# Performance work log

Measured on AMD Instinct MI355X. Metric: run time of the kernel, lower is better.

The kernel has to match this reference:

```python
import jax, jax.numpy as jnp
import numpy as np

B, S, H = 2, 2048, 2048
N = 16               # num heads
NOPE, ROPE, V = 128, 64, 128
QHD = NOPE + ROPE    # 192 per-head q/k dim
QL, KVL = 1536, 512  # q_lora_rank, kv_lora_rank
THETA = 10000.0
SCALE = QHD ** -0.5
EPS = 1e-6


def rmsnorm(x, w):
    var = jnp.mean(x.astype(jnp.float32) ** 2, axis=-1, keepdims=True)
    return (x.astype(jnp.float32) * jax.lax.rsqrt(var + EPS)).astype(x.dtype) * w


def rotate_half(x):
    d = x.shape[-1] // 2
    return jnp.concatenate([-x[..., d:], x[..., :d]], axis=-1)


def setup_inputs() -> dict:
    key = jax.random.key(0)
    ks = jax.random.split(key, 8)
    w = lambda k, shape: jax.random.normal(k, shape, jnp.float32) * 0.02
    return {
        "hidden_states": jax.random.normal(ks[0], (B, S, H), jnp.float32),
        "position_ids": (jnp.arange(B * S, dtype=jnp.int64) % 4096).reshape(B, S),
        "q_a_w": w(ks[1], (QL, H)),
        "q_a_ln_w": jnp.ones((QL,), jnp.float32),
        "q_b_w": w(ks[2], (N * QHD, QL)),
        "kv_a_w": w(ks[3], (KVL + ROPE, H)),
        "kv_a_ln_w": jnp.ones((KVL,), jnp.float32),
        "kv_b_w": w(ks[4], (N * (NOPE + V), KVL)),
        "o_w": w(ks[5], (H, N * V)),
    }


def mla_forward(hidden_states, position_ids, q_a_w, q_a_ln_w, q_b_w,
                kv_a_w, kv_a_ln_w, kv_b_w, o_w):
    b, s, _ = hidden_states.shape
    # ---- Q low-rank path: q_b(rmsnorm(q_a(x))) ----
    q = rmsnorm(hidden_states @ q_a_w.T, q_a_ln_w) @ q_b_w.T
    q = q.reshape(b, s, N, QHD)
    q_nope, q_pe = q[..., :NOPE], q[..., NOPE:]
    # ---- compressed KV + shared rope key ----
    kv_a = hidden_states @ kv_a_w.T                       # [b,s,KVL+ROPE]
    compressed_kv = rmsnorm(kv_a[..., :KVL], kv_a_ln_w)   # [b,s,KVL]
    k_pe = kv_a[..., KVL:].reshape(b, s, 1, ROPE)         # MQA rope key
    # ---- RoPE (default, theta=1e4) from position_ids ----
    inv_freq = 1.0 / (THETA ** (jnp.arange(0, ROPE, 2, dtype=jnp.float32) / ROPE))
    freqs = position_ids.astype(jnp.float32)[..., None] * inv_freq  # [b,s,ROPE/2]
    emb = jnp.concatenate([freqs, freqs], axis=-1)                  # [b,s,ROPE]
    cos = jnp.cos(emb)[:, :, None, :].astype(hidden_states.dtype)   # [b,s,1,ROPE]
    sin = jnp.sin(emb)[:, :, None, :].astype(hidden_states.dtype)
    q_pe = q_pe * cos + rotate_half(q_pe) * sin
    k_pe = k_pe * cos + rotate_half(k_pe) * sin
    # ---- decompress latent KV via kv_b_proj ----
    kv = (compressed_kv @ kv_b_w.T).reshape(b, s, N, NOPE + V)
    k_nope, v = kv[..., :NOPE], kv[..., NOPE:]
    k = jnp.concatenate([k_nope, jnp.broadcast_to(k_pe, (b, s, N, ROPE))], axis=-1)
    qf = jnp.concatenate([q_nope, q_pe], axis=-1)          # [b,s,N,QHD]
    # ---- causal SDPA in bsnd layout ----
    scores = jnp.einsum('bqnd,bknd->bnqk', qf, k) * SCALE  # [b,N,s,s]
    causal = jnp.tril(jnp.ones((s, s), bool))
    scores = jnp.where(causal, scores, jnp.finfo(scores.dtype).min)
    probs = jax.nn.softmax(scores, axis=-1)
    attn = jnp.einsum('bnqk,bknd->bqnd', probs, v)         # [b,s,N,V]
    out = attn.reshape(b, s, N * V) @ o_w.T
    return out


def reference(hidden_states, position_ids, q_a_w, q_a_ln_w, q_b_w,
              kv_a_w, kv_a_ln_w, kv_b_w, o_w):
    return mla_forward(hidden_states, position_ids, q_a_w, q_a_ln_w, q_b_w,
                       kv_a_w, kv_a_ln_w, kv_b_w, o_w)
```

## Files before the change

kernel.cpp:

```cpp
#include <hip/hip_runtime.h>
#include <cstdio>

typedef unsigned short u16;
typedef u16 u16x4 __attribute__((ext_vector_type(4)));
typedef u16 u16x8 __attribute__((ext_vector_type(8)));
typedef __bf16 bf16x8 __attribute__((ext_vector_type(8)));
typedef float f32x4 __attribute__((ext_vector_type(4)));

#define AS1 __attribute__((address_space(1)))
#define AS3 __attribute__((address_space(3)))

#define GLOAD16(gsrc, ldst) __builtin_amdgcn_global_load_lds( \
    (const AS1 void*)(gsrc), (AS3 void*)(ldst), 16, 0, 0)

__device__ __forceinline__ u16 f2bf(float f) {
  unsigned u = __builtin_bit_cast(unsigned, f);
  u += 0x7fffu + ((u >> 16) & 1u);
  return (u16)(u >> 16);
}
__device__ __forceinline__ float bf2f(u16 h) {
  return __builtin_bit_cast(float, (unsigned)h << 16);
}

__global__ __launch_bounds__(256) void cvt_pad_k(const float* __restrict__ src,
                                                 u16* __restrict__ dst,
                                                 long srcN, long dstN) {
  long i = ((long)blockIdx.x * 256 + threadIdx.x) * 8;
  const long stride = (long)gridDim.x * 256 * 8;
  for (; i < dstN; i += stride) {
    u16x8 o = {0,0,0,0,0,0,0,0};
    if (i < srcN) {
      const float4* p = (const float4*)(src + i);
      float4 a = p[0], b = p[1];
      o[0]=f2bf(a.x); o[1]=f2bf(a.y); o[2]=f2bf(a.z); o[3]=f2bf(a.w);
      o[4]=f2bf(b.x); o[5]=f2bf(b.y); o[6]=f2bf(b.z); o[7]=f2bf(b.w);
    }
    *(u16x8*)(dst + i) = o;
  }
}

__global__ __launch_bounds__(256) void rms_k(const u16* __restrict__ src, u16* __restrict__ dst,
                                             const float* __restrict__ w,
                                             int sstride, int dstride, int cols) {
  const int row = blockIdx.x;
  const int tid = threadIdx.x;
  const int nch = cols >> 3;
  float x[8];
  float ss = 0.f;
  if (tid < nch) {
    u16x8 v = *(const u16x8*)(src + (size_t)row * sstride + tid * 8);
#pragma unroll
    for (int j = 0; j < 8; ++j) { x[j] = bf2f(v[j]); ss += x[j] * x[j]; }
  } else {
#pragma unroll
    for (int j = 0; j < 8; ++j) x[j] = 0.f;
  }
#pragma unroll
  for (int off = 1; off < 64; off <<= 1) ss += __shfl_xor(ss, off);
  __shared__ float red[4];
  const int wv = tid >> 6, ln = tid & 63;
  if (ln == 0) red[wv] = ss;
  __syncthreads();
  const float tot = red[0] + red[1] + red[2] + red[3];
  const float rs = 1.0f / sqrtf(tot / (float)cols + 1e-6f);
  if (tid < nch) {
    u16x8 o;
#pragma unroll
    for (int j = 0; j < 8; ++j) o[j] = f2bf(x[j] * rs * w[tid * 8 + j]);
    *(u16x8*)(dst + (size_t)row * dstride + tid * 8) = o;
  }
}

__global__ void rope_k(u16* __restrict__ q, const u16* __restrict__ kva,
                       u16* __restrict__ kpe, const int* __restrict__ pos) {
  const int tok = blockIdx.x;
  const int j = threadIdx.x;
  const float p = (float)pos[tok];
  const int jj = j & 31;
  const float inv = __powf(10000.0f, -(float)jj * (1.0f / 32.0f));
  float s, c;
  __sincosf(p * inv, &s, &c);
  const float sgn = (j < 32) ? -1.0f : 1.0f;
  const int partner = (j < 32) ? j + 32 : j - 32;
  {
    const float x  = bf2f(kva[(size_t)tok * 640 + 512 + j]);
    const float xp = bf2f(kva[(size_t)tok * 640 + 512 + partner]);
    kpe[(size_t)tok * 64 + j] = f2bf(x * c + sgn * xp * s);
  }
#pragma unroll
  for (int h = 0; h < 16; ++h) {
    const size_t base = (size_t)tok * 3072 + h * 192 + 128;
    const float x  = bf2f(q[base + j]);
    const float xp = bf2f(q[base + partner]);
    q[base + j] = f2bf(x * c + sgn * xp * s);
  }
}

__global__ __launch_bounds__(256) void gemm_bt(const u16* __restrict__ A, const u16* __restrict__ B,
                                               u16* __restrict__ Cb, float* __restrict__ Cf,
                                               int M, int N, int K) {
  __shared__ __attribute__((aligned(16))) u16 As[128 * 64];
  __shared__ __attribute__((aligned(16))) u16 Bs[128 * 64];
  const int tid = threadIdx.x;
  const int m0 = blockIdx.y * 128, n0 = blockIdx.x * 128;
  const int w = tid >> 6, lane = tid & 63;
  const int wr = w >> 1, wc = w & 1;
  const int lr = lane & 15, g = lane >> 4;

  f32x4 acc[4][4] = {};

  for (int k0 = 0; k0 < K; k0 += 64) {
#pragma unroll
    for (int i = 0; i < 4; ++i) {
      const int c = i * 256 + tid;
      const int row = c >> 3, col = (c & 7) << 3;
      GLOAD16(A + (size_t)(m0 + row) * K + k0 + col, &As[c * 8]);
    }
#pragma unroll
    for (int i = 0; i < 4; ++i) {
      const int c = i * 256 + tid;
      const int row = c >> 3, col = (c & 7) << 3;
      GLOAD16(B + (size_t)(n0 + row) * K + k0 + col, &Bs[c * 8]);
    }
    __syncthreads();
    bf16x8 af[4][2], bfr[4][2];
#pragma unroll
    for (int x = 0; x < 4; ++x)
#pragma unroll
      for (int kk = 0; kk < 2; ++kk) {
        af[x][kk]  = *(const bf16x8*)(&As[(wr * 64 + x * 16 + lr) * 64 + kk * 32 + g * 8]);
        bfr[x][kk] = *(const bf16x8*)(&Bs[(wc * 64 + x * 16 + lr) * 64 + kk * 32 + g * 8]);
      }
#pragma unroll
    for (int mi = 0; mi < 4; ++mi)
#pragma unroll
      for (int ni = 0; ni < 4; ++ni)
#pragma unroll
        for (int kk = 0; kk < 2; ++kk)
          acc[mi][ni] = __builtin_amdgcn_mfma_f32_16x16x32_bf16(af[mi][kk], bfr[ni][kk],
                                                                acc[mi][ni], 0, 0, 0);
    __syncthreads();
  }

  const int rb = m0 + wr * 64, cb = n0 + wc * 64;
#pragma unroll
  for (int mi = 0; mi < 4; ++mi)
#pragma unroll
    for (int ni = 0; ni < 4; ++ni)
#pragma unroll
      for (int i = 0; i < 4; ++i) {
        const int r = rb + mi * 16 + g * 4 + i;
        const int cI = cb + ni * 16 + lr;
        if (Cf) Cf[(size_t)r * N + cI] = acc[mi][ni][i];
        else    Cb[(size_t)r * N + cI] = f2bf(acc[mi][ni][i]);
      }
}

__global__ __launch_bounds__(256) void attn_k(const u16* __restrict__ q, const u16* __restrict__ kvb,
                                              const u16* __restrict__ kpe, u16* __restrict__ ao) {
  __shared__ __attribute__((aligned(16))) u16 Ks[64 * 192];
  __shared__ __attribute__((aligned(16))) u16 Vt[128 * 64];
  __shared__ __attribute__((aligned(16))) u16 Ps[4][32 * 72];

  const float SCALE = 0.07216878364870323f;
  const int bh = blockIdx.x;
  const int b = bh >> 4, h = bh & 15;
  const int j = 15 - blockIdx.y;
  const int tid = threadIdx.x, w = tid >> 6, lane = tid & 63;
  const int lr = lane & 15, g = lane >> 4;

  const int q0 = j * 128;
  const int qrb = q0 + w * 32;

  bf16x8 qf[2][6];
#pragma unroll
  for (int m = 0; m < 2; ++m)
#pragma unroll
    for (int kd = 0; kd < 6; ++kd)
      qf[m][kd] = *(const bf16x8*)(q + (size_t)(b * 2048 + qrb + m * 16 + lr) * 3072 +
                                   h * 192 + kd * 32 + g * 8);

  float mrow[2][4], lrow[2][4];
  f32x4 o[2][8] = {};
#pragma unroll
  for (int m = 0; m < 2; ++m)
#pragma unroll
    for (int i = 0; i < 4; ++i) { mrow[m][i] = -1e30f; lrow[m][i] = 0.f; }

  const int nt = (q0 >> 6) + 2;
  for (int t = 0; t < nt; ++t) {
    const int k0 = t * 64;
#pragma unroll
    for (int i = 0; i < 6; ++i) {
      const int c = i * 256 + tid;
      const int row = c / 24, cl = c - row * 24;
      const int cg = cl ^ (row & 7);
      const u16* src = (cg < 16)
        ? (kvb + (size_t)(b * 2048 + k0 + row) * 4096 + h * 256 + cg * 8)
        : (kpe + (size_t)(b * 2048 + k0 + row) * 64 + (cg - 16) * 8);
      GLOAD16(src, &Ks[c * 8]);
    }
    {
      const int kq = tid >> 4;
      const int vc = (tid & 15) << 3;
      u16x8 vv[4];
#pragma unroll
      for (int r = 0; r < 4; ++r)
        vv[r] = *(const u16x8*)(kvb + (size_t)(b * 2048 + k0 + kq * 4 + r) * 4096 + h * 256 + 128 + vc);
#pragma unroll
      for (int e = 0; e < 8; ++e) {
        const int v = vc + e;
        const int cx = (kq >> 1) ^ (v & 7) ^ ((v >> 3) & 7);
        u16x4 tq = {vv[0][e], vv[1][e], vv[2][e], vv[3][e]};
        *(u16x4*)(&Vt[v * 64 + cx * 8 + (kq & 1) * 4]) = tq;
      }
    }
    __syncthreads();

    if (k0 <= qrb + 31) {
      f32x4 sAcc[2][4] = {};
#pragma unroll
      for (int nf = 0; nf < 4; ++nf) {
        const int rr = nf * 16 + lr;
#pragma unroll
        for (int kd = 0; kd < 6; ++kd) {
          const int ch = (kd * 4 + g) ^ (rr & 7);
          const bf16x8 kf = *(const bf16x8*)(&Ks[rr * 192 + ch * 8]);
#pragma unroll
          for (int m = 0; m < 2; ++m)
            sAcc[m][nf] = __builtin_amdgcn_mfma_f32_16x16x32_bf16(qf[m][kd], kf, sAcc[m][nf], 0, 0, 0);
        }
      }

#pragma unroll
      for (int m = 0; m < 2; ++m) {
        float sv[4][4];
#pragma unroll
        for (int nf = 0; nf < 4; ++nf)
#pragma unroll
          for (int i = 0; i < 4; ++i) {
            const int qrow = qrb + m * 16 + g * 4 + i;
            const int kcol = k0 + nf * 16 + lr;
            const float vS = sAcc[m][nf][i] * SCALE;
            sv[nf][i] = (kcol > qrow) ? -1e30f : vS;
          }
        float fac[4], mn[4];
#pragma unroll
        for (int i = 0; i < 4; ++i) {
          float rm = fmaxf(fmaxf(sv[0][i], sv[1][i]), fmaxf(sv[2][i], sv[3][i]));
          rm = fmaxf(rm, __shfl_xor(rm, 1));
          rm = fmaxf(rm, __shfl_xor(rm, 2));
          rm = fmaxf(rm, __shfl_xor(rm, 4));
          rm = fmaxf(rm, __shfl_xor(rm, 8));
          mn[i] = fmaxf(mrow[m][i], rm);
          fac[i] = __expf(mrow[m][i] - mn[i]);
          mrow[m][i] = mn[i];
        }
#pragma unroll
        for (int i = 0; i < 4; ++i) {
          float rsum = 0.f;
#pragma unroll
          for (int nf = 0; nf < 4; ++nf) { sv[nf][i] = __expf(sv[nf][i] - mn[i]); rsum += sv[nf][i]; }
          rsum += __shfl_xor(rsum, 1);
          rsum += __shfl_xor(rsum, 2);
          rsum += __shfl_xor(rsum, 4);
          rsum += __shfl_xor(rsum, 8);
          lrow[m][i] = lrow[m][i] * fac[i] + rsum;
        }
#pragma unroll
        for (int nv = 0; nv < 8; ++nv)
#pragma unroll
          for (int i = 0; i < 4; ++i) o[m][nv][i] *= fac[i];
#pragma unroll
        for (int nf = 0; nf < 4; ++nf)
#pragma unroll
          for (int i = 0; i < 4; ++i)
            Ps[w][(m * 16 + g * 4 + i) * 72 + nf * 16 + lr] = f2bf(sv[nf][i]);
      }
      asm volatile("s_waitcnt lgkmcnt(0)" ::: "memory");

#pragma unroll
      for (int kc = 0; kc < 2; ++kc) {
        bf16x8 vfr[8];
#pragma unroll
        for (int nv = 0; nv < 8; ++nv) {
          const int v = nv * 16 + lr;
          const int cx = (kc * 4 + g) ^ (v & 7) ^ ((v >> 3) & 7);
          vfr[nv] = *(const bf16x8*)(&Vt[v * 64 + cx * 8]);
        }
#pragma unroll
        for (int m = 0; m < 2; ++m) {
          const bf16x8 pf = *(const bf16x8*)(&Ps[w][(m * 16 + lr) * 72 + kc * 32 + g * 8]);
#pragma unroll
          for (int nv = 0; nv < 8; ++nv)
            o[m][nv] = __builtin_amdgcn_mfma_f32_16x16x32_bf16(pf, vfr[nv], o[m][nv], 0, 0, 0);
        }
      }
    }
    __syncthreads();
  }

#pragma unroll
  for (int m = 0; m < 2; ++m)
#pragma unroll
    for (int i = 0; i < 4; ++i) {
      const float inv = 1.0f / lrow[m][i];
      const size_t tokOff = (size_t)(b * 2048 + qrb + m * 16 + g * 4 + i) * 2048 + h * 128;
#pragma unroll
      for (int nv = 0; nv < 8; ++nv)
        ao[tokOff + nv * 16 + lr] = f2bf(o[m][nv][i] * inv);
    }
}

extern "C" void kernel_launch(void* const* d_in, const int* in_sizes, int n_in,
                              void* d_out, int out_size, void* d_ws, size_t ws_size,
                              hipStream_t stream) {
  const float* hidden  = (const float*)d_in[0];
  const int*   pos     = (const int*)d_in[1];
  const float* q_a_w   = (const float*)d_in[2];
  const float* q_a_ln  = (const float*)d_in[3];
  const float* q_b_w   = (const float*)d_in[4];
  const float* kv_a_w  = (const float*)d_in[5];
  const float* kv_a_ln = (const float*)d_in[6];
  const float* kv_b_w  = (const float*)d_in[7];
  const float* o_w     = (const float*)d_in[8];
  float* out = (float*)d_out;

  char* ws = (char*)d_ws;
  u16* hb  = (u16*)(ws + 0L);
  u16* w1  = (u16*)(ws + 16777216L);
  u16* w2  = (u16*)(ws + 23068672L);
  u16* w3  = (u16*)(ws + 32505856L);
  u16* w4  = (u16*)(ws + 35127296L);
  u16* w5  = (u16*)(ws + 39321600L);
  u16* qa  = (u16*)(ws + 47710208L);
  u16* qb  = (u16*)(ws + 60293120L);
  u16* kva = (u16*)(ws + 85458944L);
  u16* ckv = (u16*)(ws + 90701824L);
  u16* kpe = (u16*)(ws + 94896128L);
  u16* kvb = (u16*)(ws + 95420416L);
  u16* ao  = (u16*)(ws + 128974848L);
  if (ws_size < 145752064UL) { fprintf(stderr, "ws too small: %zu\n", ws_size); return; }

  auto cvt = [&](const float* s, u16* d, long sn, long dn) {
    long blocks = (dn / 8 + 255) / 256; if (blocks > 2048) blocks = 2048;
    cvt_pad_k<<<dim3((unsigned)blocks), dim3(256), 0, stream>>>(s, d, sn, dn);
  };
  cvt(hidden, hb, 4096L * 2048, 4096L * 2048);
  cvt(q_a_w,  w1, 1536L * 2048, 1536L * 2048);
  cvt(q_b_w,  w2, 3072L * 1536, 3072L * 1536);
  cvt(kv_a_w, w3, 576L * 2048,  640L * 2048);
  cvt(kv_b_w, w4, 4096L * 512,  4096L * 512);
  cvt(o_w,    w5, 2048L * 2048, 2048L * 2048);

  gemm_bt<<<dim3(12, 32), 256, 0, stream>>>(hb, w1, qa, nullptr, 4096, 1536, 2048);
  rms_k<<<4096, 256, 0, stream>>>(qa, qa, q_a_ln, 1536, 1536, 1536);
  gemm_bt<<<dim3(24, 32), 256, 0, stream>>>(qa, w2, qb, nullptr, 4096, 3072, 1536);
  gemm_bt<<<dim3(5, 32), 256, 0, stream>>>(hb, w3, kva, nullptr, 4096, 640, 2048);
  rms_k<<<4096, 256, 0, stream>>>(kva, ckv, kv_a_ln, 640, 512, 512);
  rope_k<<<4096, 64, 0, stream>>>(qb, kva, kpe, pos);
  gemm_bt<<<dim3(32, 32), 256, 0, stream>>>(ckv, w4, kvb, nullptr, 4096, 4096, 512);
  attn_k<<<dim3(32, 16), 256, 0, stream>>>(qb, kvb, kpe, ao);
  gemm_bt<<<dim3(16, 32), 256, 0, stream>>>(ao, w5, nullptr, out, 4096, 2048, 2048);
}
```

Before: 481.0 us.

## Register-prefetch next K/V tile in attention, lazy softmax rescale, wider rope blocks

The attention kernel now loads the next K/V tile into registers while the current tile is being computed, then writes it to LDS at the top of the next iteration. This replaces the direct global-to-LDS loads and one of the two barriers per tile, hiding global load latency behind the math. It also skips the online-softmax rescale of the output and row sum unless some row max grows by more than 8, and it asks for two blocks per SM via launch bounds. Separately, rope_k uses 256 threads per token, with the heads split across four waves. The trade-offs are more register pressure and possible spills, since the prefetch keeps ten extra 16-byte vectors live per thread.

```diff
diff --git a/kernel.cpp b/kernel.cpp
--- a/kernel.cpp
+++ b/kernel.cpp
@@ -71,10 +71,11 @@
   }
 }
 
-__global__ void rope_k(u16* __restrict__ q, const u16* __restrict__ kva,
-                       u16* __restrict__ kpe, const int* __restrict__ pos) {
+__global__ __launch_bounds__(256) void rope_k(u16* __restrict__ q, const u16* __restrict__ kva,
+                                              u16* __restrict__ kpe, const int* __restrict__ pos) {
   const int tok = blockIdx.x;
-  const int j = threadIdx.x;
+  const int j = threadIdx.x & 63;
+  const int w = threadIdx.x >> 6;
   const float p = (float)pos[tok];
   const int jj = j & 31;
   const float inv = __powf(10000.0f, -(float)jj * (1.0f / 32.0f));
@@ -82,13 +83,14 @@
   __sincosf(p * inv, &s, &c);
   const float sgn = (j < 32) ? -1.0f : 1.0f;
   const int partner = (j < 32) ? j + 32 : j - 32;
-  {
+  if (w == 0) {
     const float x  = bf2f(kva[(size_t)tok * 640 + 512 + j]);
     const float xp = bf2f(kva[(size_t)tok * 640 + 512 + partner]);
     kpe[(size_t)tok * 64 + j] = f2bf(x * c + sgn * xp * s);
   }
 #pragma unroll
-  for (int h = 0; h < 16; ++h) {
+  for (int hh = 0; hh < 4; ++hh) {
+    const int h = w * 4 + hh;
     const size_t base = (size_t)tok * 3072 + h * 192 + 128;
     const float x  = bf2f(q[base + j]);
     const float xp = bf2f(q[base + partner]);
@@ -156,8 +158,8 @@
       }
 }
 
-__global__ __launch_bounds__(256) void attn_k(const u16* __restrict__ q, const u16* __restrict__ kvb,
-                                              const u16* __restrict__ kpe, u16* __restrict__ ao) {
+__global__ __launch_bounds__(256, 2) void attn_k(const u16* __restrict__ q, const u16* __restrict__ kvb,
+                                                 const u16* __restrict__ kpe, u16* __restrict__ ao) {
   __shared__ __attribute__((aligned(16))) u16 Ks[64 * 192];
   __shared__ __attribute__((aligned(16))) u16 Vt[128 * 64];
   __shared__ __attribute__((aligned(16))) u16 Ps[4][32 * 72];
@@ -180,6 +182,34 @@
       qf[m][kd] = *(const bf16x8*)(q + (size_t)(b * 2048 + qrb + m * 16 + lr) * 3072 +
                                    h * 192 + kd * 32 + g * 8);
 
+  const u16* kptr[6];
+  int kld[6], kstep[6];
+#pragma unroll
+  for (int i = 0; i < 6; ++i) {
+    const int c = i * 256 + tid;
+    const int row = c / 24, cl = c - row * 24;
+    kld[i] = (row * 24 + (cl ^ (row & 7))) * 8;
+    if (cl < 16) { kptr[i] = kvb + (size_t)(b * 2048 + row) * 4096 + h * 256 + cl * 8;
+                   kstep[i] = 64 * 4096; }
+    else         { kptr[i] = kpe + (size_t)(b * 2048 + row) * 64 + (cl - 16) * 8;
+                   kstep[i] = 64 * 64; }
+  }
+  const int kq = tid >> 4, vc = (tid & 15) << 3;
+  const u16* vptr = kvb + (size_t)(b * 2048 + kq * 4) * 4096 + h * 256 + 128 + vc;
+  int vld[8];
+#pragma unroll
+  for (int e = 0; e < 8; ++e) {
+    const int v = vc + e;
+    const int cx = (kq >> 1) ^ (v & 7) ^ ((v >> 3) & 7);
+    vld[e] = v * 64 + cx * 8 + (kq & 1) * 4;
+  }
+
+  u16x8 kreg[6], vreg[4];
+#define LOAD_TILE() do { \
+    _Pragma("unroll") for (int i = 0; i < 6; ++i) kreg[i] = *(const u16x8*)kptr[i]; \
+    _Pragma("unroll") for (int r = 0; r < 4; ++r) vreg[r] = *(const u16x8*)(vptr + r * 4096); \
+  } while (0)
+
   float mrow[2][4], lrow[2][4];
   f32x4 o[2][8] = {};
 #pragma unroll
@@ -188,34 +218,27 @@
     for (int i = 0; i < 4; ++i) { mrow[m][i] = -1e30f; lrow[m][i] = 0.f; }
 
   const int nt = (q0 >> 6) + 2;
+  LOAD_TILE();
+
   for (int t = 0; t < nt; ++t) {
     const int k0 = t * 64;
-#pragma unroll
-    for (int i = 0; i < 6; ++i) {
-      const int c = i * 256 + tid;
-      const int row = c / 24, cl = c - row * 24;
-      const int cg = cl ^ (row & 7);
-      const u16* src = (cg < 16)
-        ? (kvb + (size_t)(b * 2048 + k0 + row) * 4096 + h * 256 + cg * 8)
-        : (kpe + (size_t)(b * 2048 + k0 + row) * 64 + (cg - 16) * 8);
-      GLOAD16(src, &Ks[c * 8]);
-    }
-    {
-      const int kq = tid >> 4;
-      const int vc = (tid & 15) << 3;
-      u16x8 vv[4];
-#pragma unroll
-      for (int r = 0; r < 4; ++r)
-        vv[r] = *(const u16x8*)(kvb + (size_t)(b * 2048 + k0 + kq * 4 + r) * 4096 + h * 256 + 128 + vc);
-#pragma unroll
-      for (int e = 0; e < 8; ++e) {
-        const int v = vc + e;
-        const int cx = (kq >> 1) ^ (v & 7) ^ ((v >> 3) & 7);
-        u16x4 tq = {vv[0][e], vv[1][e], vv[2][e], vv[3][e]};
-        *(u16x4*)(&Vt[v * 64 + cx * 8 + (kq & 1) * 4]) = tq;
-      }
-    }
-    __syncthreads();
+    __builtin_amdgcn_s_barrier();
+#pragma unroll
+    for (int i = 0; i < 6; ++i) *(u16x8*)(&Ks[kld[i]]) = kreg[i];
+#pragma unroll
+    for (int e = 0; e < 8; ++e) {
+      u16x4 tq = {vreg[0][e], vreg[1][e], vreg[2][e], vreg[3][e]};
+      *(u16x4*)(&Vt[vld[e]]) = tq;
+    }
+    if (t + 1 < nt) {
+#pragma unroll
+      for (int i = 0; i < 6; ++i) kptr[i] += kstep[i];
+      vptr += 64 * 4096;
+      LOAD_TILE();
+    }
+    asm volatile("s_waitcnt lgkmcnt(0)" ::: "memory");
+    __builtin_amdgcn_s_barrier();
+    __builtin_amdgcn_sched_barrier(0);
 
     if (k0 <= qrb + 31) {
       f32x4 sAcc[2][4] = {};
@@ -244,7 +267,8 @@
             const float vS = sAcc[m][nf][i] * SCALE;
             sv[nf][i] = (kcol > qrow) ? -1e30f : vS;
           }
-        float fac[4], mn[4];
+        float rm4[4];
+        bool exceed = false;
 #pragma unroll
         for (int i = 0; i < 4; ++i) {
           float rm = fmaxf(fmaxf(sv[0][i], sv[1][i]), fmaxf(sv[2][i], sv[3][i]));
@@ -252,25 +276,31 @@
           rm = fmaxf(rm, __shfl_xor(rm, 2));
           rm = fmaxf(rm, __shfl_xor(rm, 4));
           rm = fmaxf(rm, __shfl_xor(rm, 8));
-          mn[i] = fmaxf(mrow[m][i], rm);
-          fac[i] = __expf(mrow[m][i] - mn[i]);
-          mrow[m][i] = mn[i];
+          rm4[i] = rm;
+          exceed = exceed || (rm > mrow[m][i] + 8.0f);
+        }
+        if (__any(exceed)) {
+#pragma unroll
+          for (int i = 0; i < 4; ++i) {
+            const float mn = fmaxf(mrow[m][i], rm4[i]);
+            const float fac = __expf(mrow[m][i] - mn);
+            mrow[m][i] = mn;
+            lrow[m][i] *= fac;
+#pragma unroll
+            for (int nv = 0; nv < 8; ++nv) o[m][nv][i] *= fac;
+          }
         }
 #pragma unroll
         for (int i = 0; i < 4; ++i) {
           float rsum = 0.f;
 #pragma unroll
-          for (int nf = 0; nf < 4; ++nf) { sv[nf][i] = __expf(sv[nf][i] - mn[i]); rsum += sv[nf][i]; }
+          for (int nf = 0; nf < 4; ++nf) { sv[nf][i] = __expf(sv[nf][i] - mrow[m][i]); rsum += sv[nf][i]; }
           rsum += __shfl_xor(rsum, 1);
           rsum += __shfl_xor(rsum, 2);
           rsum += __shfl_xor(rsum, 4);
           rsum += __shfl_xor(rsum, 8);
-          lrow[m][i] = lrow[m][i] * fac[i] + rsum;
-        }
-#pragma unroll
-        for (int nv = 0; nv < 8; ++nv)
-#pragma unroll
-          for (int i = 0; i < 4; ++i) o[m][nv][i] *= fac[i];
+          lrow[m][i] += rsum;
+        }
 #pragma unroll
         for (int nf = 0; nf < 4; ++nf)
 #pragma unroll
@@ -297,8 +327,8 @@
         }
       }
     }
-    __syncthreads();
-  }
+  }
+#undef LOAD_TILE
 
 #pragma unroll
   for (int m = 0; m < 2; ++m)
@@ -358,7 +388,7 @@
   gemm_bt<<<dim3(24, 32), 256, 0, stream>>>(qa, w2, qb, nullptr, 4096, 3072, 1536);
   gemm_bt<<<dim3(5, 32), 256, 0, stream>>>(hb, w3, kva, nullptr, 4096, 640, 2048);
   rms_k<<<4096, 256, 0, stream>>>(kva, ckv, kv_a_ln, 640, 512, 512);
-  rope_k<<<4096, 64, 0, stream>>>(qb, kva, kpe, pos);
+  rope_k<<<4096, 256, 0, stream>>>(qb, kva, kpe, pos);
   gemm_bt<<<dim3(32, 32), 256, 0, stream>>>(ckv, w4, kvb, nullptr, 4096, 4096, 512);
   attn_k<<<dim3(32, 16), 256, 0, stream>>>(qb, kvb, kpe, ao);
   gemm_bt<<<dim3(16, 32), 256, 0, stream>>>(ao, w5, nullptr, out, 4096, 2048, 2048);
```

Measured after the change: 491.5 us. 2.2% more time.

## Lazy softmax rescaling in attention, reorder causal blocks, widen rope blocks

Applied to the files above, without the earlier changes.

The attention kernel now skips the online-softmax rescale of the output accumulator unless the new row max exceeds the running max by more than 8 (FA4-style lazy rescale), which removes most multiply passes over the output accumulator. The causal query-block order is changed so half the y-blocks run heavy-first and half light-first, aiming for better load balance. The rope kernel uses 256 threads per token, with each wave handling 4 heads, to raise per-block parallelism. Lazy rescaling lets exp values grow up to e^8, a small numerical risk in bf16 P.

```diff
diff --git a/kernel.cpp b/kernel.cpp
--- a/kernel.cpp
+++ b/kernel.cpp
@@ -71,10 +71,11 @@
   }
 }
 
-__global__ void rope_k(u16* __restrict__ q, const u16* __restrict__ kva,
-                       u16* __restrict__ kpe, const int* __restrict__ pos) {
+__global__ __launch_bounds__(256) void rope_k(u16* __restrict__ q, const u16* __restrict__ kva,
+                                              u16* __restrict__ kpe, const int* __restrict__ pos) {
   const int tok = blockIdx.x;
-  const int j = threadIdx.x;
+  const int j = threadIdx.x & 63;
+  const int w = threadIdx.x >> 6;
   const float p = (float)pos[tok];
   const int jj = j & 31;
   const float inv = __powf(10000.0f, -(float)jj * (1.0f / 32.0f));
@@ -82,13 +83,14 @@
   __sincosf(p * inv, &s, &c);
   const float sgn = (j < 32) ? -1.0f : 1.0f;
   const int partner = (j < 32) ? j + 32 : j - 32;
-  {
+  if (w == 0) {
     const float x  = bf2f(kva[(size_t)tok * 640 + 512 + j]);
     const float xp = bf2f(kva[(size_t)tok * 640 + 512 + partner]);
     kpe[(size_t)tok * 64 + j] = f2bf(x * c + sgn * xp * s);
   }
 #pragma unroll
-  for (int h = 0; h < 16; ++h) {
+  for (int hh = 0; hh < 4; ++hh) {
+    const int h = w * 4 + hh;
     const size_t base = (size_t)tok * 3072 + h * 192 + 128;
     const float x  = bf2f(q[base + j]);
     const float xp = bf2f(q[base + partner]);
@@ -165,7 +167,8 @@
   const float SCALE = 0.07216878364870323f;
   const int bh = blockIdx.x;
   const int b = bh >> 4, h = bh & 15;
-  const int j = 15 - blockIdx.y;
+  const int by = blockIdx.y;
+  const int j = (by < 8) ? (15 - by) : (by - 8);
   const int tid = threadIdx.x, w = tid >> 6, lane = tid & 63;
   const int lr = lane & 15, g = lane >> 4;
 
@@ -244,7 +247,8 @@
             const float vS = sAcc[m][nf][i] * SCALE;
             sv[nf][i] = (kcol > qrow) ? -1e30f : vS;
           }
-        float fac[4], mn[4];
+        float rm4[4];
+        bool exceed = false;
 #pragma unroll
         for (int i = 0; i < 4; ++i) {
           float rm = fmaxf(fmaxf(sv[0][i], sv[1][i]), fmaxf(sv[2][i], sv[3][i]));
@@ -252,25 +256,31 @@
           rm = fmaxf(rm, __shfl_xor(rm, 2));
           rm = fmaxf(rm, __shfl_xor(rm, 4));
           rm = fmaxf(rm, __shfl_xor(rm, 8));
-          mn[i] = fmaxf(mrow[m][i], rm);
-          fac[i] = __expf(mrow[m][i] - mn[i]);
-          mrow[m][i] = mn[i];
+          rm4[i] = rm;
+          exceed = exceed || (rm > mrow[m][i] + 8.0f);
+        }
+        if (__any(exceed)) {
+#pragma unroll
+          for (int i = 0; i < 4; ++i) {
+            const float mn = fmaxf(mrow[m][i], rm4[i]);
+            const float fac = __expf(mrow[m][i] - mn);
+            mrow[m][i] = mn;
+            lrow[m][i] *= fac;
+#pragma unroll
+            for (int nv = 0; nv < 8; ++nv) o[m][nv][i] *= fac;
+          }
         }
 #pragma unroll
         for (int i = 0; i < 4; ++i) {
           float rsum = 0.f;
 #pragma unroll
-          for (int nf = 0; nf < 4; ++nf) { sv[nf][i] = __expf(sv[nf][i] - mn[i]); rsum += sv[nf][i]; }
+          for (int nf = 0; nf < 4; ++nf) { sv[nf][i] = __expf(sv[nf][i] - mrow[m][i]); rsum += sv[nf][i]; }
           rsum += __shfl_xor(rsum, 1);
           rsum += __shfl_xor(rsum, 2);
           rsum += __shfl_xor(rsum, 4);
           rsum += __shfl_xor(rsum, 8);
-          lrow[m][i] = lrow[m][i] * fac[i] + rsum;
-        }
-#pragma unroll
-        for (int nv = 0; nv < 8; ++nv)
-#pragma unroll
-          for (int i = 0; i < 4; ++i) o[m][nv][i] *= fac[i];
+          lrow[m][i] += rsum;
+        }
 #pragma unroll
         for (int nf = 0; nf < 4; ++nf)
 #pragma unroll
@@ -358,7 +368,7 @@
   gemm_bt<<<dim3(24, 32), 256, 0, stream>>>(qa, w2, qb, nullptr, 4096, 3072, 1536);
   gemm_bt<<<dim3(5, 32), 256, 0, stream>>>(hb, w3, kva, nullptr, 4096, 640, 2048);
   rms_k<<<4096, 256, 0, stream>>>(kva, ckv, kv_a_ln, 640, 512, 512);
-  rope_k<<<4096, 64, 0, stream>>>(qb, kva, kpe, pos);
+  rope_k<<<4096, 256, 0, stream>>>(qb, kva, kpe, pos);
   gemm_bt<<<dim3(32, 32), 256, 0, stream>>>(ckv, w4, kvb, nullptr, 4096, 4096, 512);
   attn_k<<<dim3(32, 16), 256, 0, stream>>>(qb, kvb, kpe, ao);
   gemm_bt<<<dim3(16, 32), 256, 0, stream>>>(ao, w5, nullptr, out, 4096, 2048, 2048);
```

Result: slower. 503.2 us (+4.6%).
